# Performance work log

Hardware: AMD Instinct MI355X
Metric: run time of the kernel (lower is better)

## Reference

```python
import jax, jax.numpy as jnp
import numpy as np

N_NODES = 10000
N_EDGES = 640000
D_IN = 128
D_INTER = 128


def gcn_conv(x, edge_index, edge_weight, W, b):
    # PyG GCNConv: out = D^{-1/2} (A + I) D^{-1/2} (X W) + b
    n = x.shape[0]
    h = x @ W  # [N, D_out]
    row, col = edge_index[0], edge_index[1]  # source, target
    loop = jnp.arange(n, dtype=row.dtype)
    row = jnp.concatenate([row, loop])
    col = jnp.concatenate([col, loop])
    ew = jnp.concatenate([edge_weight, jnp.ones((n,), edge_weight.dtype)])
    deg = jax.ops.segment_sum(ew, col, num_segments=n)  # in-degree incl. self loops
    dinv = jnp.where(deg > 0, jax.lax.rsqrt(deg), jnp.zeros_like(deg))
    norm = dinv[row] * ew * dinv[col]  # [E+N]
    msgs = norm[:, None] * h[row]  # gather + scale
    out = jax.ops.segment_sum(msgs, col, num_segments=n)  # scatter-add aggregate
    return out + b


def setup_inputs() -> dict:
    key = jax.random.key(0)
    ks = jax.random.split(key, 8)
    x = jax.random.normal(ks[0], (N_NODES, D_IN), dtype=jnp.float32)
    edge_index = jax.random.randint(ks[1], (2, N_EDGES), 0, N_NODES, dtype=jnp.int64)
    edge_weight = jax.random.uniform(ks[2], (N_EDGES,), dtype=jnp.float32)
    # Glorot-ish init for linear weights, zeros for bias (PyG default)
    s1 = 1.0 / np.sqrt(D_IN)
    s2 = 1.0 / np.sqrt(D_INTER)
    W1 = jax.random.uniform(ks[3], (D_IN, D_INTER), jnp.float32, -s1, s1)
    b1 = jnp.zeros((D_INTER,), jnp.float32)
    W2 = jax.random.uniform(ks[4], (D_INTER, D_IN), jnp.float32, -s2, s2)
    b2 = jnp.zeros((D_IN,), jnp.float32)
    return {"x": x, "edge_index": edge_index, "edge_weight": edge_weight,
            "W1": W1, "b1": b1, "W2": W2, "b2": b2}


def reference(x, edge_index, edge_weight, W1, b1, W2, b2):
    # GCN.forward in eval mode: dropout is identity
    h = jax.nn.relu(gcn_conv(x, edge_index, edge_weight, W1, b1))
    out = jax.nn.relu(gcn_conv(h, edge_index, edge_weight, W2, b2))
    return out
```

## Files before the change

kernel.cpp:

```cpp
#include <hip/hip_runtime.h>

#define NN 10000
#define NE 640000
#define D  128
#define PAD_SHIFT 7
#define GEMM_BLOCKS ((NN + 31) / 32)


__global__ __launch_bounds__(256) void zero_kernel(int* __restrict__ p, int n) {
    int i = blockIdx.x * 256 + threadIdx.x;
    if (i < n) p[i] = 0;
}


__global__ __launch_bounds__(256) void fused_gemm_count_kernel(const float* __restrict__ X,
                                                               const float* __restrict__ W,
                                                               float* __restrict__ H,
                                                               const int* __restrict__ ei,
                                                               int* __restrict__ cnt,
                                                               int* __restrict__ rank) {
    int bid = blockIdx.x;
    if (bid < GEMM_BLOCKS) {
        __shared__ float xs[32][D];
        int t  = threadIdx.x;
        int d  = t & 127;
        int rh = t >> 7;
        int r0 = bid * 32;
#pragma unroll
        for (int r = 0; r < 16; ++r) {
            int rr = r0 + rh * 16 + r;
            xs[rh * 16 + r][d] = (rr < NN) ? X[(size_t)rr * D + d] : 0.0f;
        }
        __syncthreads();
        float acc[16];
#pragma unroll
        for (int r = 0; r < 16; ++r) acc[r] = 0.0f;
        for (int k = 0; k < D; k += 4) {
            float w0 = W[(k + 0) * D + d];
            float w1 = W[(k + 1) * D + d];
            float w2 = W[(k + 2) * D + d];
            float w3 = W[(k + 3) * D + d];
#pragma unroll
            for (int r = 0; r < 16; ++r) {
                float4 xv = *reinterpret_cast<const float4*>(&xs[rh * 16 + r][k]);
                acc[r] = fmaf(xv.x, w0, acc[r]);
                acc[r] = fmaf(xv.y, w1, acc[r]);
                acc[r] = fmaf(xv.z, w2, acc[r]);
                acc[r] = fmaf(xv.w, w3, acc[r]);
            }
        }
#pragma unroll
        for (int r = 0; r < 16; ++r) {
            int rr = r0 + rh * 16 + r;
            if (rr < NN) H[(size_t)rr * D + d] = acc[r];
        }
    } else {
        int e = (bid - GEMM_BLOCKS) * 256 + threadIdx.x;
        if (e < NE) {
            int c = ei[NE + e];
            rank[e] = atomicAdd(&cnt[c], 1);
        }
    }
}


__global__ __launch_bounds__(256) void scatter_kernel(const int* __restrict__ ei,
                                                      const float* __restrict__ ew,
                                                      const int* __restrict__ rank,
                                                      int2* __restrict__ epack) {
    int e = blockIdx.x * 256 + threadIdx.x;
    if (e < NE) {
        int2 v;
        v.x = ei[e];
        v.y = __float_as_int(ew[e]);
        int c = ei[NE + e];
        epack[((size_t)c << PAD_SHIFT) + rank[e]] = v;
    }
}


__global__ __launch_bounds__(256) void degdinv_kernel(const int* __restrict__ cnt,
                                                      const int2* __restrict__ epack,
                                                      float* __restrict__ dinv) {
    int node = blockIdx.x * 4 + (threadIdx.x >> 6);
    if (node >= NN) return;
    int lane = threadIdx.x & 63;
    int m = cnt[node];
    const int2* base = epack + ((size_t)node << PAD_SHIFT);
    float s = 0.0f;
    for (int j = lane; j < m; j += 64) s += __int_as_float(base[j].y);
#pragma unroll
    for (int off = 32; off; off >>= 1) s += __shfl_down(s, off);
    if (lane == 0) dinv[node] = rsqrtf(s + 1.0f);
}


__global__ __launch_bounds__(256) void gemm_kernel(const float* __restrict__ X,
                                                   const float* __restrict__ W,
                                                   float* __restrict__ H) {
    __shared__ float xs[32][D];
    int t  = threadIdx.x;
    int d  = t & 127;
    int rh = t >> 7;
    int r0 = blockIdx.x * 32;
#pragma unroll
    for (int r = 0; r < 16; ++r) {
        int rr = r0 + rh * 16 + r;
        xs[rh * 16 + r][d] = (rr < NN) ? X[(size_t)rr * D + d] : 0.0f;
    }
    __syncthreads();
    float acc[16];
#pragma unroll
    for (int r = 0; r < 16; ++r) acc[r] = 0.0f;
    for (int k = 0; k < D; k += 4) {
        float w0 = W[(k + 0) * D + d];
        float w1 = W[(k + 1) * D + d];
        float w2 = W[(k + 2) * D + d];
        float w3 = W[(k + 3) * D + d];
#pragma unroll
        for (int r = 0; r < 16; ++r) {
            float4 xv = *reinterpret_cast<const float4*>(&xs[rh * 16 + r][k]);
            acc[r] = fmaf(xv.x, w0, acc[r]);
            acc[r] = fmaf(xv.y, w1, acc[r]);
            acc[r] = fmaf(xv.z, w2, acc[r]);
            acc[r] = fmaf(xv.w, w3, acc[r]);
        }
    }
#pragma unroll
    for (int r = 0; r < 16; ++r) {
        int rr = r0 + rh * 16 + r;
        if (rr < NN) H[(size_t)rr * D + d] = acc[r];
    }
}


__global__ __launch_bounds__(256) void agg_kernel(const float* __restrict__ H,
                                                  const int* __restrict__ cnt,
                                                  const int2* __restrict__ epack,
                                                  const float* __restrict__ dinv,
                                                  const float* __restrict__ bias,
                                                  float* __restrict__ out) {
    int node = blockIdx.x * 8 + (threadIdx.x >> 5);
    if (node >= NN) return;
    int q = threadIdx.x & 31;
    int m = cnt[node];
    const int2* eb = epack + ((size_t)node << PAD_SHIFT);
    const float4* Hq = reinterpret_cast<const float4*>(H) + q;
    float di = dinv[node];

    float4 hc = Hq[(size_t)node * 32];
    float4 acc;
    acc.x = di * hc.x; acc.y = di * hc.y; acc.z = di * hc.z; acc.w = di * hc.w;

    int j = 0;
    for (; j + 8 <= m; j += 8) {
        int   s[8];
        float n[8];
#pragma unroll
        for (int k = 0; k < 8; ++k) {
            int2 v = eb[j + k];
            s[k] = v.x;
            n[k] = dinv[v.x] * __int_as_float(v.y);
        }
#pragma unroll
        for (int k = 0; k < 8; ++k) {
            float4 hv = Hq[(size_t)s[k] * 32];
            acc.x = fmaf(n[k], hv.x, acc.x);
            acc.y = fmaf(n[k], hv.y, acc.y);
            acc.z = fmaf(n[k], hv.z, acc.z);
            acc.w = fmaf(n[k], hv.w, acc.w);
        }
    }
    for (; j < m; ++j) {
        int2 v = eb[j];
        float nn = dinv[v.x] * __int_as_float(v.y);
        float4 hv = Hq[(size_t)v.x * 32];
        acc.x = fmaf(nn, hv.x, acc.x);
        acc.y = fmaf(nn, hv.y, acc.y);
        acc.z = fmaf(nn, hv.z, acc.z);
        acc.w = fmaf(nn, hv.w, acc.w);
    }

    float4 b4 = reinterpret_cast<const float4*>(bias)[q];
    float4 o;
    o.x = fmaxf(fmaf(di, acc.x, b4.x), 0.f);
    o.y = fmaxf(fmaf(di, acc.y, b4.y), 0.f);
    o.z = fmaxf(fmaf(di, acc.z, b4.z), 0.f);
    o.w = fmaxf(fmaf(di, acc.w, b4.w), 0.f);
    reinterpret_cast<float4*>(out)[(size_t)node * 32 + q] = o;
}


extern "C" void kernel_launch(void* const* d_in, const int* in_sizes, int n_in,
                              void* d_out, int out_size, void* d_ws, size_t ws_size,
                              hipStream_t stream) {
    const float* x  = (const float*)d_in[0];
    const int*   ei = (const int*)  d_in[1];
    const float* ew = (const float*)d_in[2];
    const float* W1 = (const float*)d_in[3];
    const float* b1 = (const float*)d_in[4];
    const float* W2 = (const float*)d_in[5];
    const float* b2 = (const float*)d_in[6];
    float* out = (float*)d_out;

    char* ws = (char*)d_ws;
    size_t off = 0;
    auto alloc = [&](size_t bytes) {
        void* p = ws + off;
        off = (off + bytes + 255) & ~(size_t)255;
        return p;
    };
    int*   cnt   = (int*)  alloc(NN * 4);
    float* dinv  = (float*)alloc(NN * 4);
    int*   rank  = (int*)  alloc((size_t)NE * 4);
    int2*  epack = (int2*) alloc(((size_t)NN << PAD_SHIFT) * 8);
    float* h     = (float*)alloc((size_t)NN * D * 4);
    float* g     = (float*)alloc((size_t)NN * D * 4);

    zero_kernel<<<(NN + 255) / 256, 256, 0, stream>>>(cnt, NN);
    fused_gemm_count_kernel<<<GEMM_BLOCKS + (NE + 255) / 256, 256, 0, stream>>>(
        x, W1, h, ei, cnt, rank);
    scatter_kernel<<<(NE + 255) / 256, 256, 0, stream>>>(ei, ew, rank, epack);
    degdinv_kernel<<<(NN + 3) / 4, 256, 0, stream>>>(cnt, epack, dinv);

    agg_kernel <<<(NN + 7) / 8, 256, 0, stream>>>(h, cnt, epack, dinv, b1, g);
    gemm_kernel<<<(NN + 31) / 32, 256, 0, stream>>>(g, W2, h);
    agg_kernel <<<(NN + 7) / 8, 256, 0, stream>>>(h, cnt, epack, dinv, b2, out);
}
```

Measured before the change: 158.2 us.

## Privatize in-degree counters per XCC to make count atomics local

Edge counting now uses eight counter arrays, one per XCC, picked by reading the hardware XCC_ID register. The atomics use workgroup scope, so they stay in that XCC's own L2 instead of going device-wide. A new base_kernel turns the per-XCC counts into offsets and totals, and the scatter adds the XCC offset to the local rank. This aims to cut the cost of cross-die atomic traffic, at the price of an extra launch, a larger zeroing pass, and reliance on workgroup-scope atomics staying coherent within one XCC's L2.

```diff
diff --git a/kernel.cpp b/kernel.cpp
--- a/kernel.cpp
+++ b/kernel.cpp
@@ -5,6 +5,13 @@
 #define D  128
 #define PAD_SHIFT 7
 #define GEMM_BLOCKS ((NN + 31) / 32)
+#define CSTRIDE 10240
+
+__device__ __forceinline__ int xcc_id() {
+    unsigned x;
+    asm volatile("s_getreg_b32 %0, hwreg(HW_REG_XCC_ID)" : "=s"(x));
+    return (int)(x & 7);
+}
 
 
 __global__ __launch_bounds__(256) void zero_kernel(int* __restrict__ p, int n) {
@@ -17,7 +24,7 @@
                                                                const float* __restrict__ W,
                                                                float* __restrict__ H,
                                                                const int* __restrict__ ei,
-                                                               int* __restrict__ cnt,
+                                                               int* __restrict__ cnt8,
                                                                int* __restrict__ rank) {
     int bid = blockIdx.x;
     if (bid < GEMM_BLOCKS) {
@@ -58,23 +65,46 @@
         int e = (bid - GEMM_BLOCKS) * 256 + threadIdx.x;
         if (e < NE) {
             int c = ei[NE + e];
-            rank[e] = atomicAdd(&cnt[c], 1);
-        }
-    }
+            int x = xcc_id();
+            int lr = __hip_atomic_fetch_add(&cnt8[x * CSTRIDE + c], 1,
+                                            __ATOMIC_RELAXED,
+                                            __HIP_MEMORY_SCOPE_WORKGROUP);
+            rank[e] = (x << 16) | lr;
+        }
+    }
+}
+
+
+__global__ __launch_bounds__(256) void base_kernel(int* __restrict__ cnt8,
+                                                   int* __restrict__ cnt) {
+    int n = blockIdx.x * 256 + threadIdx.x;
+    if (n >= NN) return;
+    int b = 0;
+#pragma unroll
+    for (int x = 0; x < 8; ++x) {
+        int t = cnt8[x * CSTRIDE + n];
+        cnt8[x * CSTRIDE + n] = b;
+        b += t;
+    }
+    cnt[n] = b;
 }
 
 
 __global__ __launch_bounds__(256) void scatter_kernel(const int* __restrict__ ei,
                                                       const float* __restrict__ ew,
                                                       const int* __restrict__ rank,
+                                                      const int* __restrict__ base8,
                                                       int2* __restrict__ epack) {
     int e = blockIdx.x * 256 + threadIdx.x;
     if (e < NE) {
+        int c  = ei[NE + e];
+        int rk = rank[e];
+        int x  = rk >> 16;
+        int lr = rk & 0xFFFF;
         int2 v;
         v.x = ei[e];
         v.y = __float_as_int(ew[e]);
-        int c = ei[NE + e];
-        epack[((size_t)c << PAD_SHIFT) + rank[e]] = v;
+        epack[((size_t)c << PAD_SHIFT) + base8[x * CSTRIDE + c] + lr] = v;
     }
 }
 
@@ -210,6 +240,7 @@
         off = (off + bytes + 255) & ~(size_t)255;
         return p;
     };
+    int*   cnt8  = (int*)  alloc(8 * CSTRIDE * 4);
     int*   cnt   = (int*)  alloc(NN * 4);
     float* dinv  = (float*)alloc(NN * 4);
     int*   rank  = (int*)  alloc((size_t)NE * 4);
@@ -217,10 +248,11 @@
     float* h     = (float*)alloc((size_t)NN * D * 4);
     float* g     = (float*)alloc((size_t)NN * D * 4);
 
-    zero_kernel<<<(NN + 255) / 256, 256, 0, stream>>>(cnt, NN);
+    zero_kernel<<<(8 * CSTRIDE + 255) / 256, 256, 0, stream>>>(cnt8, 8 * CSTRIDE);
     fused_gemm_count_kernel<<<GEMM_BLOCKS + (NE + 255) / 256, 256, 0, stream>>>(
-        x, W1, h, ei, cnt, rank);
-    scatter_kernel<<<(NE + 255) / 256, 256, 0, stream>>>(ei, ew, rank, epack);
+        x, W1, h, ei, cnt8, rank);
+    base_kernel   <<<(NN + 255) / 256, 256, 0, stream>>>(cnt8, cnt);
+    scatter_kernel<<<(NE + 255) / 256, 256, 0, stream>>>(ei, ew, rank, cnt8, epack);
     degdinv_kernel<<<(NN + 3) / 4, 256, 0, stream>>>(cnt, epack, dinv);
 
     agg_kernel <<<(NN + 7) / 8, 256, 0, stream>>>(h, cnt, epack, dinv, b1, g);
```

Result: faster. 146.3 us (-7.5%).

## Replace global atomic edge counting with per-block shared-memory histograms and prefix bases

Applied to the files above, without the earlier changes.

Edge counting by target node now happens in 16 large blocks that each build a shared-memory histogram with LDS atomics, instead of one global atomicAdd per edge. A new base kernel prefix-sums the per-block histograms to produce per-block offsets and total counts, and the scatter adds base plus local rank. This removes the zero kernel and global atomic contention. The fused GEMM blocks are resized to 1024 threads with 4 rows per thread. The trade-off is that only 16 blocks do the histogram work, which may serialize and leave the GPU underused, plus an extra kernel launch.

```diff
diff --git a/kernel.cpp b/kernel.cpp
--- a/kernel.cpp
+++ b/kernel.cpp
@@ -4,45 +4,44 @@
 #define NE 640000
 #define D  128
 #define PAD_SHIFT 7
+#define B_HIST 16
+#define EPB (NE / B_HIST)
+#define HSTRIDE 10240
 #define GEMM_BLOCKS ((NN + 31) / 32)
 
 
-__global__ __launch_bounds__(256) void zero_kernel(int* __restrict__ p, int n) {
-    int i = blockIdx.x * 256 + threadIdx.x;
-    if (i < n) p[i] = 0;
-}
-
-
-__global__ __launch_bounds__(256) void fused_gemm_count_kernel(const float* __restrict__ X,
+union UShared {
+    float xs[32][D];
+    int   lh[HSTRIDE];
+};
+
+__global__ __launch_bounds__(1024) void fused_gemm_hist_kernel(const float* __restrict__ X,
                                                                const float* __restrict__ W,
                                                                float* __restrict__ H,
                                                                const int* __restrict__ ei,
-                                                               int* __restrict__ cnt,
-                                                               int* __restrict__ rank) {
+                                                               int* __restrict__ hist,
+                                                               int* __restrict__ lrank) {
+    __shared__ UShared u;
     int bid = blockIdx.x;
+    int t   = threadIdx.x;
     if (bid < GEMM_BLOCKS) {
-        __shared__ float xs[32][D];
-        int t  = threadIdx.x;
         int d  = t & 127;
-        int rh = t >> 7;
+        int rg = t >> 7;
         int r0 = bid * 32;
-#pragma unroll
-        for (int r = 0; r < 16; ++r) {
-            int rr = r0 + rh * 16 + r;
-            xs[rh * 16 + r][d] = (rr < NN) ? X[(size_t)rr * D + d] : 0.0f;
+        for (int r = rg; r < 32; r += 8) {
+            int rr = r0 + r;
+            u.xs[r][d] = (rr < NN) ? X[(size_t)rr * D + d] : 0.0f;
         }
         __syncthreads();
-        float acc[16];
-#pragma unroll
-        for (int r = 0; r < 16; ++r) acc[r] = 0.0f;
+        float acc[4] = {0.f, 0.f, 0.f, 0.f};
         for (int k = 0; k < D; k += 4) {
             float w0 = W[(k + 0) * D + d];
             float w1 = W[(k + 1) * D + d];
             float w2 = W[(k + 2) * D + d];
             float w3 = W[(k + 3) * D + d];
 #pragma unroll
-            for (int r = 0; r < 16; ++r) {
-                float4 xv = *reinterpret_cast<const float4*>(&xs[rh * 16 + r][k]);
+            for (int r = 0; r < 4; ++r) {
+                float4 xv = *reinterpret_cast<const float4*>(&u.xs[rg * 4 + r][k]);
                 acc[r] = fmaf(xv.x, w0, acc[r]);
                 acc[r] = fmaf(xv.y, w1, acc[r]);
                 acc[r] = fmaf(xv.z, w2, acc[r]);
@@ -50,31 +49,63 @@
             }
         }
 #pragma unroll
-        for (int r = 0; r < 16; ++r) {
-            int rr = r0 + rh * 16 + r;
+        for (int r = 0; r < 4; ++r) {
+            int rr = r0 + rg * 4 + r;
             if (rr < NN) H[(size_t)rr * D + d] = acc[r];
         }
     } else {
-        int e = (bid - GEMM_BLOCKS) * 256 + threadIdx.x;
-        if (e < NE) {
-            int c = ei[NE + e];
-            rank[e] = atomicAdd(&cnt[c], 1);
-        }
-    }
+        int bh = bid - GEMM_BLOCKS;
+        for (int i = t; i < HSTRIDE; i += 1024) u.lh[i] = 0;
+        __syncthreads();
+        int e0 = bh * EPB;
+        for (int kb = 0; kb < 5; ++kb) {
+            int idx[8], cc[8];
+#pragma unroll
+            for (int j = 0; j < 8; ++j) {
+                int el = t + (kb * 8 + j) * 1024;
+                idx[j] = (el < EPB) ? el : -1;
+                cc[j]  = (idx[j] >= 0) ? ei[NE + e0 + idx[j]] : 0;
+            }
+#pragma unroll
+            for (int j = 0; j < 8; ++j) {
+                if (idx[j] >= 0)
+                    lrank[e0 + idx[j]] = atomicAdd(&u.lh[cc[j]], 1);
+            }
+        }
+        __syncthreads();
+        for (int i = t; i < NN; i += 1024) hist[bh * HSTRIDE + i] = u.lh[i];
+    }
+}
+
+
+__global__ __launch_bounds__(256) void base_kernel(int* __restrict__ hist,
+                                                   int* __restrict__ cnt) {
+    int n = blockIdx.x * 256 + threadIdx.x;
+    if (n >= NN) return;
+    int b = 0;
+#pragma unroll
+    for (int x = 0; x < B_HIST; ++x) {
+        int tc = hist[x * HSTRIDE + n];
+        hist[x * HSTRIDE + n] = b;
+        b += tc;
+    }
+    cnt[n] = b;
 }
 
 
 __global__ __launch_bounds__(256) void scatter_kernel(const int* __restrict__ ei,
                                                       const float* __restrict__ ew,
-                                                      const int* __restrict__ rank,
+                                                      const int* __restrict__ lrank,
+                                                      const int* __restrict__ base,
                                                       int2* __restrict__ epack) {
     int e = blockIdx.x * 256 + threadIdx.x;
     if (e < NE) {
+        int c = ei[NE + e];
+        int b = e / EPB;
         int2 v;
         v.x = ei[e];
         v.y = __float_as_int(ew[e]);
-        int c = ei[NE + e];
-        epack[((size_t)c << PAD_SHIFT) + rank[e]] = v;
+        epack[((size_t)c << PAD_SHIFT) + base[b * HSTRIDE + c] + lrank[e]] = v;
     }
 }
 
@@ -210,17 +241,18 @@
         off = (off + bytes + 255) & ~(size_t)255;
         return p;
     };
+    int*   hist  = (int*)  alloc((size_t)B_HIST * HSTRIDE * 4);
     int*   cnt   = (int*)  alloc(NN * 4);
     float* dinv  = (float*)alloc(NN * 4);
-    int*   rank  = (int*)  alloc((size_t)NE * 4);
+    int*   lrank = (int*)  alloc((size_t)NE * 4);
     int2*  epack = (int2*) alloc(((size_t)NN << PAD_SHIFT) * 8);
     float* h     = (float*)alloc((size_t)NN * D * 4);
     float* g     = (float*)alloc((size_t)NN * D * 4);
 
-    zero_kernel<<<(NN + 255) / 256, 256, 0, stream>>>(cnt, NN);
-    fused_gemm_count_kernel<<<GEMM_BLOCKS + (NE + 255) / 256, 256, 0, stream>>>(
-        x, W1, h, ei, cnt, rank);
-    scatter_kernel<<<(NE + 255) / 256, 256, 0, stream>>>(ei, ew, rank, epack);
+    fused_gemm_hist_kernel<<<GEMM_BLOCKS + B_HIST, 1024, 0, stream>>>(
+        x, W1, h, ei, hist, lrank);
+    base_kernel   <<<(NN + 255) / 256, 256, 0, stream>>>(hist, cnt);
+    scatter_kernel<<<(NE + 255) / 256, 256, 0, stream>>>(ei, ew, lrank, hist, epack);
     degdinv_kernel<<<(NN + 3) / 4, 256, 0, stream>>>(cnt, epack, dinv);
 
     agg_kernel <<<(NN + 7) / 8, 256, 0, stream>>>(h, cnt, epack, dinv, b1, g);
```

Result: slower. 534.9 us (+238.1%).

## Replace global atomic edge counting with per-block shared histograms; one-block-per-node aggregation

Applied to the files above, without the earlier changes.

Edge ranking no longer uses global atomics. Each of 1024 blocks builds a shared-memory histogram of target nodes over its slice of edges and stores byte-sized local ranks and per-block counts. A new base kernel then walks the 1024 histogram planes serially for each node to produce per-block offsets and degree counts. The aggregation kernel also changes to one 128-thread block per node: neighbour indices and norms are staged in shared memory and each thread accumulates one feature column. The serial 1024-step prefix loop over global memory is latency-bound and may cost more than the global atomics it replaces, and the byte-sized counts assume in-degrees stay below 256.

```diff
diff --git a/kernel.cpp b/kernel.cpp
--- a/kernel.cpp
+++ b/kernel.cpp
@@ -5,31 +5,33 @@
 #define D  128
 #define PAD_SHIFT 7
 #define GEMM_BLOCKS ((NN + 31) / 32)
-
-
-__global__ __launch_bounds__(256) void zero_kernel(int* __restrict__ p, int n) {
-    int i = blockIdx.x * 256 + threadIdx.x;
-    if (i < n) p[i] = 0;
-}
-
-
-__global__ __launch_bounds__(256) void fused_gemm_count_kernel(const float* __restrict__ X,
-                                                               const float* __restrict__ W,
-                                                               float* __restrict__ H,
-                                                               const int* __restrict__ ei,
-                                                               int* __restrict__ cnt,
-                                                               int* __restrict__ rank) {
+#define NB_HIST 1024
+#define EPB (NE / NB_HIST)
+#define HSTRIDE 10240
+
+
+union UShared {
+    float xs[32][D];
+    int   lh[HSTRIDE];
+};
+
+__global__ __launch_bounds__(256) void fused_gemm_hist_kernel(const float* __restrict__ X,
+                                                              const float* __restrict__ W,
+                                                              float* __restrict__ H,
+                                                              const int* __restrict__ ei,
+                                                              unsigned char* __restrict__ hist8,
+                                                              unsigned char* __restrict__ lrank) {
+    __shared__ UShared u;
     int bid = blockIdx.x;
+    int t   = threadIdx.x;
     if (bid < GEMM_BLOCKS) {
-        __shared__ float xs[32][D];
-        int t  = threadIdx.x;
         int d  = t & 127;
         int rh = t >> 7;
         int r0 = bid * 32;
 #pragma unroll
         for (int r = 0; r < 16; ++r) {
             int rr = r0 + rh * 16 + r;
-            xs[rh * 16 + r][d] = (rr < NN) ? X[(size_t)rr * D + d] : 0.0f;
+            u.xs[rh * 16 + r][d] = (rr < NN) ? X[(size_t)rr * D + d] : 0.0f;
         }
         __syncthreads();
         float acc[16];
@@ -42,7 +44,7 @@
             float w3 = W[(k + 3) * D + d];
 #pragma unroll
             for (int r = 0; r < 16; ++r) {
-                float4 xv = *reinterpret_cast<const float4*>(&xs[rh * 16 + r][k]);
+                float4 xv = *reinterpret_cast<const float4*>(&u.xs[rh * 16 + r][k]);
                 acc[r] = fmaf(xv.x, w0, acc[r]);
                 acc[r] = fmaf(xv.y, w1, acc[r]);
                 acc[r] = fmaf(xv.z, w2, acc[r]);
@@ -55,26 +57,58 @@
             if (rr < NN) H[(size_t)rr * D + d] = acc[r];
         }
     } else {
-        int e = (bid - GEMM_BLOCKS) * 256 + threadIdx.x;
-        if (e < NE) {
-            int c = ei[NE + e];
-            rank[e] = atomicAdd(&cnt[c], 1);
-        }
-    }
+        int bh = bid - GEMM_BLOCKS;
+        int e0 = bh * EPB;
+        for (int i = t; i < HSTRIDE; i += 256) u.lh[i] = 0;
+        __syncthreads();
+        for (int j = t; j < EPB; j += 256) {
+            int c = ei[NE + e0 + j];
+            int old = atomicAdd(&u.lh[c], 1);
+            lrank[e0 + j] = (unsigned char)old;
+        }
+        __syncthreads();
+        uchar4* plane = reinterpret_cast<uchar4*>(hist8 + (size_t)bh * HSTRIDE);
+        for (int i = t; i < HSTRIDE / 4; i += 256) {
+            uchar4 v;
+            v.x = (unsigned char)u.lh[i * 4 + 0];
+            v.y = (unsigned char)u.lh[i * 4 + 1];
+            v.z = (unsigned char)u.lh[i * 4 + 2];
+            v.w = (unsigned char)u.lh[i * 4 + 3];
+            plane[i] = v;
+        }
+    }
+}
+
+
+__global__ __launch_bounds__(256) void base_kernel(unsigned char* __restrict__ hist8,
+                                                   int* __restrict__ cnt) {
+    int n = blockIdx.x * 256 + threadIdx.x;
+    if (n >= NN) return;
+    int run = 0;
+    for (int x = 0; x < NB_HIST; ++x) {
+        size_t idx = (size_t)x * HSTRIDE + n;
+        int c = hist8[idx];
+        hist8[idx] = (unsigned char)run;
+        run += c;
+    }
+    cnt[n] = run;
 }
 
 
 __global__ __launch_bounds__(256) void scatter_kernel(const int* __restrict__ ei,
                                                       const float* __restrict__ ew,
-                                                      const int* __restrict__ rank,
+                                                      const unsigned char* __restrict__ lrank,
+                                                      const unsigned char* __restrict__ base8,
                                                       int2* __restrict__ epack) {
     int e = blockIdx.x * 256 + threadIdx.x;
     if (e < NE) {
+        int c = ei[NE + e];
+        int x = e / EPB;
+        int slot = (int)base8[(size_t)x * HSTRIDE + c] + (int)lrank[e];
         int2 v;
         v.x = ei[e];
         v.y = __float_as_int(ew[e]);
-        int c = ei[NE + e];
-        epack[((size_t)c << PAD_SHIFT) + rank[e]] = v;
+        epack[((size_t)c << PAD_SHIFT) + slot] = v;
     }
 }
 
@@ -134,60 +168,35 @@
 }
 
 
-__global__ __launch_bounds__(256) void agg_kernel(const float* __restrict__ H,
-                                                  const int* __restrict__ cnt,
-                                                  const int2* __restrict__ epack,
-                                                  const float* __restrict__ dinv,
-                                                  const float* __restrict__ bias,
-                                                  float* __restrict__ out) {
-    int node = blockIdx.x * 8 + (threadIdx.x >> 5);
-    if (node >= NN) return;
-    int q = threadIdx.x & 31;
-    int m = cnt[node];
-    const int2* eb = epack + ((size_t)node << PAD_SHIFT);
-    const float4* Hq = reinterpret_cast<const float4*>(H) + q;
-    float di = dinv[node];
-
-    float4 hc = Hq[(size_t)node * 32];
-    float4 acc;
-    acc.x = di * hc.x; acc.y = di * hc.y; acc.z = di * hc.z; acc.w = di * hc.w;
-
-    int j = 0;
-    for (; j + 8 <= m; j += 8) {
-        int   s[8];
-        float n[8];
-#pragma unroll
-        for (int k = 0; k < 8; ++k) {
-            int2 v = eb[j + k];
-            s[k] = v.x;
-            n[k] = dinv[v.x] * __int_as_float(v.y);
-        }
-#pragma unroll
-        for (int k = 0; k < 8; ++k) {
-            float4 hv = Hq[(size_t)s[k] * 32];
-            acc.x = fmaf(n[k], hv.x, acc.x);
-            acc.y = fmaf(n[k], hv.y, acc.y);
-            acc.z = fmaf(n[k], hv.z, acc.z);
-            acc.w = fmaf(n[k], hv.w, acc.w);
-        }
-    }
-    for (; j < m; ++j) {
-        int2 v = eb[j];
-        float nn = dinv[v.x] * __int_as_float(v.y);
-        float4 hv = Hq[(size_t)v.x * 32];
-        acc.x = fmaf(nn, hv.x, acc.x);
-        acc.y = fmaf(nn, hv.y, acc.y);
-        acc.z = fmaf(nn, hv.z, acc.z);
-        acc.w = fmaf(nn, hv.w, acc.w);
-    }
-
-    float4 b4 = reinterpret_cast<const float4*>(bias)[q];
-    float4 o;
-    o.x = fmaxf(fmaf(di, acc.x, b4.x), 0.f);
-    o.y = fmaxf(fmaf(di, acc.y, b4.y), 0.f);
-    o.z = fmaxf(fmaf(di, acc.z, b4.z), 0.f);
-    o.w = fmaxf(fmaf(di, acc.w, b4.w), 0.f);
-    reinterpret_cast<float4*>(out)[(size_t)node * 32 + q] = o;
+__global__ __launch_bounds__(128) void agg_feat_kernel(const float* __restrict__ H,
+                                                       const int* __restrict__ cnt,
+                                                       const int2* __restrict__ epack,
+                                                       const float* __restrict__ dinv,
+                                                       const float* __restrict__ bias,
+                                                       float* __restrict__ out) {
+    __shared__ int   s_src[128];
+    __shared__ float s_n[128];
+    int c = blockIdx.x;
+    int d = threadIdx.x;
+    int m = cnt[c];
+    const int2* eb = epack + ((size_t)c << PAD_SHIFT);
+    float di = dinv[c];
+    if (d < m) {
+        int2 v = eb[d];
+        s_src[d] = v.x;
+        s_n[d]   = dinv[v.x] * __int_as_float(v.y);
+    }
+    __syncthreads();
+    float acc = di * H[(size_t)c * D + d];
+    int jj = 0;
+    for (; jj + 8 <= m; jj += 8) {
+#pragma unroll
+        for (int k = 0; k < 8; ++k)
+            acc = fmaf(s_n[jj + k], H[(size_t)s_src[jj + k] * D + d], acc);
+    }
+    for (; jj < m; ++jj)
+        acc = fmaf(s_n[jj], H[(size_t)s_src[jj] * D + d], acc);
+    out[(size_t)c * D + d] = fmaxf(fmaf(di, acc, bias[d]), 0.0f);
 }
 
 
@@ -210,20 +219,21 @@
         off = (off + bytes + 255) & ~(size_t)255;
         return p;
     };
+    unsigned char* hist8 = (unsigned char*)alloc((size_t)NB_HIST * HSTRIDE);
+    unsigned char* lrank = (unsigned char*)alloc((size_t)NE);
     int*   cnt   = (int*)  alloc(NN * 4);
     float* dinv  = (float*)alloc(NN * 4);
-    int*   rank  = (int*)  alloc((size_t)NE * 4);
     int2*  epack = (int2*) alloc(((size_t)NN << PAD_SHIFT) * 8);
     float* h     = (float*)alloc((size_t)NN * D * 4);
     float* g     = (float*)alloc((size_t)NN * D * 4);
 
-    zero_kernel<<<(NN + 255) / 256, 256, 0, stream>>>(cnt, NN);
-    fused_gemm_count_kernel<<<GEMM_BLOCKS + (NE + 255) / 256, 256, 0, stream>>>(
-        x, W1, h, ei, cnt, rank);
-    scatter_kernel<<<(NE + 255) / 256, 256, 0, stream>>>(ei, ew, rank, epack);
+    fused_gemm_hist_kernel<<<GEMM_BLOCKS + NB_HIST, 256, 0, stream>>>(
+        x, W1, h, ei, hist8, lrank);
+    base_kernel   <<<40, 256, 0, stream>>>(hist8, cnt);
+    scatter_kernel<<<(NE + 255) / 256, 256, 0, stream>>>(ei, ew, lrank, hist8, epack);
     degdinv_kernel<<<(NN + 3) / 4, 256, 0, stream>>>(cnt, epack, dinv);
 
-    agg_kernel <<<(NN + 7) / 8, 256, 0, stream>>>(h, cnt, epack, dinv, b1, g);
-    gemm_kernel<<<(NN + 31) / 32, 256, 0, stream>>>(g, W2, h);
-    agg_kernel <<<(NN + 7) / 8, 256, 0, stream>>>(h, cnt, epack, dinv, b2, out);
-}
+    agg_feat_kernel<<<NN, 128, 0, stream>>>(h, cnt, epack, dinv, b1, g);
+    gemm_kernel    <<<(NN + 31) / 32, 256, 0, stream>>>(g, W2, h);
+    agg_feat_kernel<<<NN, 128, 0, stream>>>(h, cnt, epack, dinv, b2, out);
+}
```

After: 156.1 us. No clear change (-1.3%).
